# Optimization experiments

Measured on AMD Instinct MI355X. Metric: run time of the kernel, lower is better.

## Reference

```python
import jax, jax.numpy as jnp
import numpy as np

N_NODES = 50000
N_EDGES = 800000
H = 128   # atom_hidden_feats
B = 64    # bond_in_feats
NEG_SLOPE = 0.01  # torch LeakyReLU default


def setup_inputs() -> dict:
    key = jax.random.key(0)
    k1, k2, k3, k4, k5 = jax.random.split(key, 5)
    feat = jax.random.normal(k1, (N_NODES, H), dtype=jnp.float32)
    gdf_feat = jax.random.normal(k2, (N_EDGES, B), dtype=jnp.float32)
    # Linear(2H+B -> H): weight [H, 2H+B], bias [H]
    W = jax.random.normal(k3, (H, 2 * H + B), dtype=jnp.float32) * 0.05
    b = jnp.zeros((H,), dtype=jnp.float32)
    src = jax.random.randint(k4, (N_EDGES,), 0, N_NODES, dtype=jnp.int64)
    dst = jax.random.randint(k5, (N_EDGES,), 0, N_NODES, dtype=jnp.int64)
    return {"feat": feat, "gdf_feat": gdf_feat, "W": W, "b": b, "src": src, "dst": dst}


def reference(feat, gdf_feat, W, b, src, dst):
    n_nodes = feat.shape[0]
    # Per-edge message: concat(src_feat, dst_feat, edge_feat) -> linear -> gate
    z = jnp.concatenate([feat[src], feat[dst], gdf_feat], axis=-1)  # [E, 2H+B]
    z = z @ W.T + b                                                 # [E, H]
    msg = jax.nn.sigmoid(z) * jnp.where(z > 0, z, NEG_SLOPE * z)    # sigmoid * leaky_relu
    # Scatter-sum messages to destination nodes
    return jax.ops.segment_sum(msg, dst, num_segments=n_nodes)      # [N, H]
```

## Files before the change

### kernel.cpp

```cpp
#include <hip/hip_runtime.h>
#include <hip/hip_bf16.h>

typedef __attribute__((ext_vector_type(8)))  short bf16x8;
typedef __attribute__((ext_vector_type(16))) float f32x16;
typedef __attribute__((ext_vector_type(4)))  float f32x4;
typedef __attribute__((ext_vector_type(2)))  __fp16 fp16x2;

#define NN 50000
#define EE 800000
#define HH 128
#define KK 320
#define NEG 0.01f
#define NTILES (EE / 64)
#define NBLK 768
#define NSB 196

#define ACC_BYTES   ((size_t)NN * HH * 2)
#define FEATB_BYTES ((size_t)NN * HH * 2)
#define PERM_BYTES  ((size_t)EE * 4)
#define CNT_BYTES   ((size_t)50176 * 4)

__device__ __forceinline__ unsigned pack2(float a, float b) {
    unsigned short lo = __builtin_bit_cast(unsigned short, __float2bfloat16(a));
    unsigned short hi = __builtin_bit_cast(unsigned short, __float2bfloat16(b));
    return (unsigned)lo | ((unsigned)hi << 16);
}

__global__ __launch_bounds__(256) void featcvt_kernel(const float* __restrict__ feat,
                                                      ushort* __restrict__ featb)
{
    const int t = blockIdx.x * 256 + threadIdx.x;
    const float* p = feat + (long long)t * 8;
    f32x4 v0 = *(const f32x4*)p;
    f32x4 v1 = *(const f32x4*)(p + 4);
    int4 h;
    h.x = (int)pack2(v0[0], v0[1]); h.y = (int)pack2(v0[2], v0[3]);
    h.z = (int)pack2(v1[0], v1[1]); h.w = (int)pack2(v1[2], v1[3]);
    *(int4*)(featb + (long long)t * 8) = h;
}

__global__ __launch_bounds__(256) void hist_kernel(const int* __restrict__ dst,
                                                   unsigned* __restrict__ cnt)
{
    const int e = blockIdx.x * 256 + threadIdx.x;
    atomicAdd(&cnt[dst[e]], 1u);
}

__global__ __launch_bounds__(256) void scan1_kernel(const unsigned* __restrict__ cnt,
                                                    unsigned* __restrict__ base,
                                                    unsigned* __restrict__ bsum)
{
    __shared__ unsigned s[256];
    const int tid = threadIdx.x;
    const int g = blockIdx.x * 256 + tid;
    unsigned v = (g < NN) ? cnt[g] : 0u;
    s[tid] = v; __syncthreads();
    #pragma unroll
    for (int o = 1; o < 256; o <<= 1) {
        unsigned t = (tid >= o) ? s[tid - o] : 0u;
        __syncthreads();
        if (tid >= o) s[tid] += t;
        __syncthreads();
    }
    if (g < NN) base[g] = s[tid] - v;
    if (tid == 255) bsum[blockIdx.x] = s[255];
}

__global__ __launch_bounds__(256) void scan2_kernel(unsigned* __restrict__ bsum)
{
    __shared__ unsigned s[256];
    const int tid = threadIdx.x;
    unsigned v = (tid < NSB) ? bsum[tid] : 0u;
    s[tid] = v; __syncthreads();
    #pragma unroll
    for (int o = 1; o < 256; o <<= 1) {
        unsigned t = (tid >= o) ? s[tid - o] : 0u;
        __syncthreads();
        if (tid >= o) s[tid] += t;
        __syncthreads();
    }
    if (tid < NSB) bsum[tid] = s[tid] - v;
}

__global__ __launch_bounds__(256) void scan3_kernel(unsigned* __restrict__ base,
                                                    const unsigned* __restrict__ bsum)
{
    const int g = blockIdx.x * 256 + threadIdx.x;
    if (g < NN) base[g] += bsum[blockIdx.x];
}

__global__ __launch_bounds__(256) void permbuild_kernel(const int* __restrict__ dst,
                                                        const unsigned* __restrict__ base,
                                                        unsigned* __restrict__ cursor,
                                                        int* __restrict__ perm)
{
    const int e = blockIdx.x * 256 + threadIdx.x;
    const int d = dst[e];
    const unsigned rank = atomicAdd(&cursor[d], 1u);
    perm[base[d] + rank] = e;
}

__global__ __launch_bounds__(256, 3) void fused_sorted_kernel(
    const ushort* __restrict__ featb, const float* __restrict__ gdf,
    const float*  __restrict__ W,     const float* __restrict__ bias,
    const int*    __restrict__ src,   const int*   __restrict__ dst,
    const int*    __restrict__ perm,  __fp16* __restrict__ acc16)
{
    __shared__ char lds[64 * 640];
    __shared__ int  dsts[64];

    const int tid  = threadIdx.x;
    const int lane = tid & 63;
    const int wid  = tid >> 6;
    const int col  = wid * 32 + (lane & 31);
    const int khalf = lane >> 5;
    const int r = tid >> 2, q = tid & 3;

    bf16x8 Wb[20];
    {
        const float* wrow = W + col * KK + khalf * 8;
        #pragma unroll
        for (int k = 0; k < 20; k++) {
            f32x4 x0 = *(const f32x4*)(wrow + k * 16);
            f32x4 x1 = *(const f32x4*)(wrow + k * 16 + 4);
            union { bf16x8 v; unsigned u[4]; } t;
            t.u[0] = pack2(x0[0], x0[1]); t.u[1] = pack2(x0[2], x0[3]);
            t.u[2] = pack2(x1[0], x1[1]); t.u[3] = pack2(x1[2], x1[3]);
            Wb[k] = t.v;
        }
    }
    const float bv = bias[col];

    const int xcd = blockIdx.x & 7, wI = blockIdx.x >> 3;
    const int cid = xcd * (NBLK / 8) + wI;
    const int qc  = NTILES / NBLK;
    const int rem = NTILES % NBLK;
    const int t0  = cid * qc + (cid < rem ? cid : rem);
    const int len = qc + (cid < rem ? 1 : 0);

    int eCur, sCur, dCur;
    {
        const long long p = (long long)t0 * 64 + r;
        eCur = perm[p]; sCur = src[eCur]; dCur = dst[eCur];
    }

    const int arow = lane & 31;
    const int xa   = (arow & 7) << 4;

    auto flush = [&](int dn, float v) {
        const float o = __shfl_xor(v, 1);
        if (!(lane & 1)) {
            fp16x2 hv = __builtin_amdgcn_cvt_pkrtz(v, o);
            __fp16* pa = acc16 + (long long)dn * HH + col;
            asm volatile("global_atomic_pk_add_f16 %0, %1, off"
                         :: "v"(pa), "v"(hv) : "memory");
        }
    };

    for (int t = t0; t < t0 + len; ++t) {
        if (q == 0) dsts[r] = dCur;
        {
            const ushort* fs = featb + (long long)sCur * HH;
            const ushort* fd = featb + (long long)dCur * HH;
            const float*  ge = gdf + (long long)eCur * 64;
            const int xr = (r & 7) << 4;
            #pragma unroll
            for (int i = 0; i < 8; i++) {
                const int c = q + i * 4;
                int4 h = *(const int4*)((c < 16) ? (fs + c * 8) : (fd + (c - 16) * 8));
                *(int4*)(lds + r * 640 + ((c * 16) ^ xr)) = h;
            }
            #pragma unroll
            for (int i = 8; i < 10; i++) {
                const int c = q + i * 4;
                const float* p = ge + (c - 32) * 8;
                f32x4 v0 = *(const f32x4*)p;
                f32x4 v1 = *(const f32x4*)(p + 4);
                int4 h;
                h.x = (int)pack2(v0[0], v0[1]); h.y = (int)pack2(v0[2], v0[3]);
                h.z = (int)pack2(v1[0], v1[1]); h.w = (int)pack2(v1[2], v1[3]);
                *(int4*)(lds + r * 640 + ((c * 16) ^ xr)) = h;
            }
        }
        if (t + 1 < t0 + len) {
            const long long p = (long long)(t + 1) * 64 + r;
            eCur = perm[p]; sCur = src[eCur]; dCur = dst[eCur];
        }
        __syncthreads();

        f32x16 acc0 = {}; f32x16 acc1 = {};
        #pragma unroll
        for (int k = 0; k < 20; k++) {
            const int kb = k * 32 + khalf * 16;
            bf16x8 a0 = *(const bf16x8*)(lds + arow * 640 + (kb ^ xa));
            bf16x8 a1 = *(const bf16x8*)(lds + (arow + 32) * 640 + (kb ^ xa));
            acc0 = __builtin_amdgcn_mfma_f32_32x32x16_bf16(a0, Wb[k], acc0, 0, 0, 0);
            acc1 = __builtin_amdgcn_mfma_f32_32x32x16_bf16(a1, Wb[k], acc1, 0, 0, 0);
        }

        #pragma unroll
        for (int rt = 0; rt < 2; rt++) {
            const f32x16 A = rt ? acc1 : acc0;
            #pragma unroll
            for (int g = 0; g < 4; g++) {
                const int4 dn4 = *(const int4*)(&dsts[rt * 32 + g * 8 + khalf * 4]);
                const int dd[4] = { dn4.x, dn4.y, dn4.z, dn4.w };
                float mm[4];
                #pragma unroll
                for (int j = 0; j < 4; j++) {
                    const float z  = A[g * 4 + j] + bv;
                    const float lr = z > 0.f ? z : NEG * z;
                    mm[j] = lr / (1.f + __expf(-z));
                }
                float s = mm[0];
                #pragma unroll
                for (int j = 1; j < 4; j++) {
                    if (dd[j] == dd[j - 1]) s += mm[j];
                    else { flush(dd[j - 1], s); s = mm[j]; }
                }
                flush(dd[3], s);
            }
        }
        __syncthreads();
    }
}

__global__ __launch_bounds__(256) void conv_kernel(const int4* __restrict__ acc,
                                                   float4* __restrict__ out)
{
    const int i = blockIdx.x * 256 + threadIdx.x;
    union { int4 v; __fp16 h[8]; } u;
    u.v = acc[i];
    float4 a, b;
    a.x = (float)u.h[0]; a.y = (float)u.h[1]; a.z = (float)u.h[2]; a.w = (float)u.h[3];
    b.x = (float)u.h[4]; b.y = (float)u.h[5]; b.z = (float)u.h[6]; b.w = (float)u.h[7];
    out[2 * i]     = a;
    out[2 * i + 1] = b;
}

__global__ __launch_bounds__(256) void fused_fallback_kernel(
    const float* __restrict__ feat, const float* __restrict__ gdf,
    const float* __restrict__ W,    const float* __restrict__ bias,
    const int*   __restrict__ src,  const int*   __restrict__ dst,
    float* __restrict__ out)
{
    __shared__ int4 lds4[64 * 40];
    __shared__ int  dsts[64];
    char* lds = (char*)lds4;
    const int tid = threadIdx.x, lane = tid & 63, wid = tid >> 6;
    const int col = wid * 32 + (lane & 31), khalf = lane >> 5;
    const int r = tid >> 2, q = tid & 3;
    const long long ebase = (long long)blockIdx.x * 64;

    bf16x8 Wb[20];
    {
        const float* wrow = W + col * KK + khalf * 8;
        #pragma unroll
        for (int k = 0; k < 20; k++) {
            f32x4 x0 = *(const f32x4*)(wrow + k * 16);
            f32x4 x1 = *(const f32x4*)(wrow + k * 16 + 4);
            union { bf16x8 v; unsigned u[4]; } t;
            t.u[0] = pack2(x0[0], x0[1]); t.u[1] = pack2(x0[2], x0[3]);
            t.u[2] = pack2(x1[0], x1[1]); t.u[3] = pack2(x1[2], x1[3]);
            Wb[k] = t.v;
        }
    }
    const int s = src[ebase + r], d = dst[ebase + r];
    if (q == 0) dsts[r] = d;
    {
        const float* fs = feat + (long long)s * HH;
        const float* fd = feat + (long long)d * HH;
        const float* ge = gdf + (ebase + r) * 64;
        #pragma unroll
        for (int i = 0; i < 10; i++) {
            const int c = q + i * 4;
            const float* p = (c < 16) ? (fs + c * 8)
                           : (c < 32) ? (fd + (c - 16) * 8)
                                      : (ge + (c - 32) * 8);
            f32x4 v0 = *(const f32x4*)p;
            f32x4 v1 = *(const f32x4*)(p + 4);
            int4 h;
            h.x = (int)pack2(v0[0], v0[1]); h.y = (int)pack2(v0[2], v0[3]);
            h.z = (int)pack2(v1[0], v1[1]); h.w = (int)pack2(v1[2], v1[3]);
            *(int4*)(lds + r * 640 + ((c * 16) ^ ((r & 7) << 4))) = h;
        }
    }
    __syncthreads();
    f32x16 acc0 = {}; f32x16 acc1 = {};
    const int arow = lane & 31, xa = (arow & 7) << 4;
    #pragma unroll
    for (int k = 0; k < 20; k++) {
        const int kb = k * 32 + khalf * 16;
        bf16x8 a0 = *(const bf16x8*)(lds + arow * 640 + (kb ^ xa));
        bf16x8 a1 = *(const bf16x8*)(lds + (arow + 32) * 640 + (kb ^ xa));
        acc0 = __builtin_amdgcn_mfma_f32_32x32x16_bf16(a0, Wb[k], acc0, 0, 0, 0);
        acc1 = __builtin_amdgcn_mfma_f32_32x32x16_bf16(a1, Wb[k], acc1, 0, 0, 0);
    }
    const float bv = bias[col];
    #pragma unroll
    for (int rt = 0; rt < 2; rt++) {
        const f32x16 A = rt ? acc1 : acc0;
        #pragma unroll
        for (int g = 0; g < 4; g++) {
            #pragma unroll
            for (int j = 0; j < 4; j++) {
                const int reg = g * 4 + j;
                const int row = j + g * 8 + khalf * 4;
                const float z  = A[reg] + bv;
                const float lr = z > 0.f ? z : NEG * z;
                const float sgm = 1.f / (1.f + __expf(-z));
                unsafeAtomicAdd(out + (long long)dsts[rt * 32 + row] * HH + col, lr * sgm);
            }
        }
    }
}

extern "C" void kernel_launch(void* const* d_in, const int* in_sizes, int n_in,
                              void* d_out, int out_size, void* d_ws, size_t ws_size,
                              hipStream_t stream) {
    const float* feat = (const float*)d_in[0];
    const float* gdf  = (const float*)d_in[1];
    const float* W    = (const float*)d_in[2];
    const float* bias = (const float*)d_in[3];
    const int*   src  = (const int*)d_in[4];
    const int*   dst  = (const int*)d_in[5];
    float* out = (float*)d_out;

    char* wsb = (char*)d_ws;
    __fp16*   acc16  = (__fp16*)wsb;
    ushort*   featb  = (ushort*)(wsb + ACC_BYTES);
    int*      perm   = (int*)(wsb + ACC_BYTES + FEATB_BYTES);
    unsigned* cnt    = (unsigned*)(wsb + ACC_BYTES + FEATB_BYTES + PERM_BYTES);
    unsigned* base   = cnt + 50176;
    unsigned* cursor = base + 50176;
    unsigned* bsum   = cursor + 50176;
    const size_t fullBytes = ACC_BYTES + FEATB_BYTES + PERM_BYTES + 3 * CNT_BYTES + 4096;

    if (ws_size >= fullBytes) {
        (void)hipMemsetAsync(acc16, 0, ACC_BYTES, stream);
        (void)hipMemsetAsync(cnt, 0, CNT_BYTES, stream);
        (void)hipMemsetAsync(cursor, 0, CNT_BYTES + 4096, stream);
        featcvt_kernel<<<NN * HH / 8 / 256, 256, 0, stream>>>(feat, featb);
        hist_kernel<<<EE / 256, 256, 0, stream>>>(dst, cnt);
        scan1_kernel<<<NSB, 256, 0, stream>>>(cnt, base, bsum);
        scan2_kernel<<<1, 256, 0, stream>>>(bsum);
        scan3_kernel<<<NSB, 256, 0, stream>>>(base, bsum);
        permbuild_kernel<<<EE / 256, 256, 0, stream>>>(dst, base, cursor, perm);
        fused_sorted_kernel<<<NBLK, 256, 0, stream>>>(featb, gdf, W, bias,
                                                      src, dst, perm, acc16);
        conv_kernel<<<NN * HH / 8 / 256, 256, 0, stream>>>((const int4*)acc16,
                                                           (float4*)out);
    } else {
        (void)hipMemsetAsync(out, 0, (size_t)out_size * sizeof(float), stream);
        fused_fallback_kernel<<<EE / 64, 256, 0, stream>>>(feat, gdf, W, bias,
                                                           src, dst, out);
    }
}
```

Baseline: 359.9 us.

## Double-buffer edge tile staging and fuse histogram into feature conversion

The main sorted kernel now issues the global gathers for the next 64-edge tile into registers before running the MFMA loop on the current tile. It then writes them to LDS after the MFMAs, with a double-buffered destination index array, so gather latency overlaps compute. The histogram kernel is folded into the feature conversion kernel, since both have 800000 threads, and two memsets are merged into one, cutting launches. In exchange the kernel holds more registers for staged data, which may lower occupancy, and the single LDS tile buffer relies on barrier ordering for correctness.

```diff
diff --git a/kernel.cpp b/kernel.cpp
--- a/kernel.cpp
+++ b/kernel.cpp
@@ -26,8 +26,10 @@
     return (unsigned)lo | ((unsigned)hi << 16);
 }
 
-__global__ __launch_bounds__(256) void featcvt_kernel(const float* __restrict__ feat,
-                                                      ushort* __restrict__ featb)
+__global__ __launch_bounds__(256) void cvt_hist_kernel(const float* __restrict__ feat,
+                                                       ushort* __restrict__ featb,
+                                                       const int* __restrict__ dst,
+                                                       unsigned* __restrict__ cnt)
 {
     const int t = blockIdx.x * 256 + threadIdx.x;
     const float* p = feat + (long long)t * 8;
@@ -37,13 +39,7 @@
     h.x = (int)pack2(v0[0], v0[1]); h.y = (int)pack2(v0[2], v0[3]);
     h.z = (int)pack2(v1[0], v1[1]); h.w = (int)pack2(v1[2], v1[3]);
     *(int4*)(featb + (long long)t * 8) = h;
-}
-
-__global__ __launch_bounds__(256) void hist_kernel(const int* __restrict__ dst,
-                                                   unsigned* __restrict__ cnt)
-{
-    const int e = blockIdx.x * 256 + threadIdx.x;
-    atomicAdd(&cnt[dst[e]], 1u);
+    atomicAdd(&cnt[dst[t]], 1u);
 }
 
 __global__ __launch_bounds__(256) void scan1_kernel(const unsigned* __restrict__ cnt,
@@ -107,7 +103,7 @@
     const int*    __restrict__ perm,  __fp16* __restrict__ acc16)
 {
     __shared__ char lds[64 * 640];
-    __shared__ int  dsts[64];
+    __shared__ int  dsts[2][64];
 
     const int tid  = threadIdx.x;
     const int lane = tid & 63;
@@ -137,16 +133,47 @@
     const int rem = NTILES % NBLK;
     const int t0  = cid * qc + (cid < rem ? cid : rem);
     const int len = qc + (cid < rem ? 1 : 0);
-
-    int eCur, sCur, dCur;
-    {
-        const long long p = (long long)t0 * 64 + r;
-        eCur = perm[p]; sCur = src[eCur]; dCur = dst[eCur];
-    }
-
-    const int arow = lane & 31;
-    const int xa   = (arow & 7) << 4;
-
+    const int tEnd = t0 + len;
+
+    int4  sf[8];
+    f32x4 sgv[4];
+    int   dStage;
+
+    auto issueLoads = [&](int e_i, int s_i, int d_i) {
+        const ushort* fs = featb + (long long)s_i * HH;
+        const ushort* fd = featb + (long long)d_i * HH;
+        const float*  ge = gdf + (long long)e_i * 64;
+        #pragma unroll
+        for (int i = 0; i < 8; i++) {
+            const int c = q + i * 4;
+            sf[i] = *(const int4*)((c < 16) ? (fs + c * 8) : (fd + (c - 16) * 8));
+        }
+        #pragma unroll
+        for (int i = 0; i < 2; i++) {
+            const int cg = q + i * 4;
+            sgv[2 * i]     = *(const f32x4*)(ge + cg * 8);
+            sgv[2 * i + 1] = *(const f32x4*)(ge + cg * 8 + 4);
+        }
+    };
+    auto writeStage = [&](int buf) {
+        const int xr = (r & 7) << 4;
+        #pragma unroll
+        for (int i = 0; i < 8; i++) {
+            const int c = q + i * 4;
+            *(int4*)(lds + r * 640 + ((c * 16) ^ xr)) = sf[i];
+        }
+        #pragma unroll
+        for (int i = 0; i < 2; i++) {
+            const int c = 32 + q + i * 4;
+            int4 h;
+            h.x = (int)pack2(sgv[2*i][0], sgv[2*i][1]);
+            h.y = (int)pack2(sgv[2*i][2], sgv[2*i][3]);
+            h.z = (int)pack2(sgv[2*i+1][0], sgv[2*i+1][1]);
+            h.w = (int)pack2(sgv[2*i+1][2], sgv[2*i+1][3]);
+            *(int4*)(lds + r * 640 + ((c * 16) ^ xr)) = h;
+        }
+        if (q == 0) dsts[buf][r] = dStage;
+    };
     auto flush = [&](int dn, float v) {
         const float o = __shfl_xor(v, 1);
         if (!(lane & 1)) {
@@ -157,36 +184,36 @@
         }
     };
 
-    for (int t = t0; t < t0 + len; ++t) {
-        if (q == 0) dsts[r] = dCur;
-        {
-            const ushort* fs = featb + (long long)sCur * HH;
-            const ushort* fd = featb + (long long)dCur * HH;
-            const float*  ge = gdf + (long long)eCur * 64;
-            const int xr = (r & 7) << 4;
-            #pragma unroll
-            for (int i = 0; i < 8; i++) {
-                const int c = q + i * 4;
-                int4 h = *(const int4*)((c < 16) ? (fs + c * 8) : (fd + (c - 16) * 8));
-                *(int4*)(lds + r * 640 + ((c * 16) ^ xr)) = h;
+    int eA, sA, dA;
+    {
+        const long long p = (long long)t0 * 64 + r;
+        eA = perm[p]; sA = src[eA]; dA = dst[eA];
+    }
+    issueLoads(eA, sA, dA);
+    dStage = dA;
+    if (len > 1) {
+        const long long p = (long long)(t0 + 1) * 64 + r;
+        eA = perm[p]; sA = src[eA]; dA = dst[eA];
+    }
+    writeStage(0);
+    asm volatile("s_waitcnt lgkmcnt(0)" ::: "memory");
+    __builtin_amdgcn_sched_barrier(0);
+    __builtin_amdgcn_s_barrier();
+
+    const int arow = lane & 31;
+    const int xa   = (arow & 7) << 4;
+    int cur = 0;
+
+    for (int t = t0; ; ++t) {
+        const bool hasNext = (t + 1 < tEnd);
+        if (hasNext) {
+            issueLoads(eA, sA, dA);
+            dStage = dA;
+            if (t + 2 < tEnd) {
+                const long long p = (long long)(t + 2) * 64 + r;
+                eA = perm[p]; sA = src[eA]; dA = dst[eA];
             }
-            #pragma unroll
-            for (int i = 8; i < 10; i++) {
-                const int c = q + i * 4;
-                const float* p = ge + (c - 32) * 8;
-                f32x4 v0 = *(const f32x4*)p;
-                f32x4 v1 = *(const f32x4*)(p + 4);
-                int4 h;
-                h.x = (int)pack2(v0[0], v0[1]); h.y = (int)pack2(v0[2], v0[3]);
-                h.z = (int)pack2(v1[0], v1[1]); h.w = (int)pack2(v1[2], v1[3]);
-                *(int4*)(lds + r * 640 + ((c * 16) ^ xr)) = h;
-            }
-        }
-        if (t + 1 < t0 + len) {
-            const long long p = (long long)(t + 1) * 64 + r;
-            eCur = perm[p]; sCur = src[eCur]; dCur = dst[eCur];
-        }
-        __syncthreads();
+        }
 
         f32x16 acc0 = {}; f32x16 acc1 = {};
         #pragma unroll
@@ -198,12 +225,21 @@
             acc1 = __builtin_amdgcn_mfma_f32_32x32x16_bf16(a1, Wb[k], acc1, 0, 0, 0);
         }
 
+        if (hasNext) {
+            __builtin_amdgcn_s_barrier();
+            __builtin_amdgcn_sched_barrier(0);
+            writeStage(cur ^ 1);
+            asm volatile("s_waitcnt lgkmcnt(0)" ::: "memory");
+            __builtin_amdgcn_sched_barrier(0);
+            __builtin_amdgcn_s_barrier();
+        }
+
         #pragma unroll
         for (int rt = 0; rt < 2; rt++) {
             const f32x16 A = rt ? acc1 : acc0;
             #pragma unroll
             for (int g = 0; g < 4; g++) {
-                const int4 dn4 = *(const int4*)(&dsts[rt * 32 + g * 8 + khalf * 4]);
+                const int4 dn4 = *(const int4*)(&dsts[cur][rt * 32 + g * 8 + khalf * 4]);
                 const int dd[4] = { dn4.x, dn4.y, dn4.z, dn4.w };
                 float mm[4];
                 #pragma unroll
@@ -221,7 +257,9 @@
                 flush(dd[3], s);
             }
         }
-        __syncthreads();
+
+        if (!hasNext) break;
+        cur ^= 1;
     }
 }
 
@@ -331,17 +369,16 @@
     ushort*   featb  = (ushort*)(wsb + ACC_BYTES);
     int*      perm   = (int*)(wsb + ACC_BYTES + FEATB_BYTES);
     unsigned* cnt    = (unsigned*)(wsb + ACC_BYTES + FEATB_BYTES + PERM_BYTES);
-    unsigned* base   = cnt + 50176;
-    unsigned* cursor = base + 50176;
+    unsigned* cursor = cnt + 50176;
     unsigned* bsum   = cursor + 50176;
-    const size_t fullBytes = ACC_BYTES + FEATB_BYTES + PERM_BYTES + 3 * CNT_BYTES + 4096;
+    unsigned* base   = bsum + 1024;
+    const size_t fullBytes = ACC_BYTES + FEATB_BYTES + PERM_BYTES
+                           + 2 * CNT_BYTES + 4096 + CNT_BYTES;
 
     if (ws_size >= fullBytes) {
         (void)hipMemsetAsync(acc16, 0, ACC_BYTES, stream);
-        (void)hipMemsetAsync(cnt, 0, CNT_BYTES, stream);
-        (void)hipMemsetAsync(cursor, 0, CNT_BYTES + 4096, stream);
-        featcvt_kernel<<<NN * HH / 8 / 256, 256, 0, stream>>>(feat, featb);
-        hist_kernel<<<EE / 256, 256, 0, stream>>>(dst, cnt);
+        (void)hipMemsetAsync(cnt, 0, 2 * CNT_BYTES + 4096, stream);
+        cvt_hist_kernel<<<NN * HH / 8 / 256, 256, 0, stream>>>(feat, featb, dst, cnt);
         scan1_kernel<<<NSB, 256, 0, stream>>>(cnt, base, bsum);
         scan2_kernel<<<1, 256, 0, stream>>>(bsum);
         scan3_kernel<<<NSB, 256, 0, stream>>>(base, bsum);
```

After: 440.3 us. +22.3%, slower.

## Double-buffer async LDS tile loads and atomically accumulate fp32 directly into output

Applied to the files above, without the earlier changes.

The sorted fused kernel is rewritten to work on 32-edge tiles. Each tile's feature rows are prefetched with global_load_lds into a double-buffered LDS area while the current tile runs on MFMA, and index lookups are pipelined several tiles ahead. The fp16 packed-atomic accumulator, its memset, the run-merging of equal destinations and the final conversion kernel are removed; messages are now added straight into the fp32 output with per-element atomics. The feature conversion and the destination histogram are also merged into a single kernel. In exchange the kernel issues more global atomics per edge, because consecutive same-destination messages are no longer combined and fp32 atomics replace packed fp16 ones.

```diff
diff --git a/kernel.cpp b/kernel.cpp
--- a/kernel.cpp
+++ b/kernel.cpp
@@ -4,46 +4,45 @@
 typedef __attribute__((ext_vector_type(8)))  short bf16x8;
 typedef __attribute__((ext_vector_type(16))) float f32x16;
 typedef __attribute__((ext_vector_type(4)))  float f32x4;
-typedef __attribute__((ext_vector_type(2)))  __fp16 fp16x2;
 
 #define NN 50000
 #define EE 800000
 #define HH 128
 #define KK 320
 #define NEG 0.01f
-#define NTILES (EE / 64)
+#define TROWS 32
+#define NT2 (EE / TROWS)
 #define NBLK 768
 #define NSB 196
 
-#define ACC_BYTES   ((size_t)NN * HH * 2)
 #define FEATB_BYTES ((size_t)NN * HH * 2)
 #define PERM_BYTES  ((size_t)EE * 4)
-#define CNT_BYTES   ((size_t)50176 * 4)
-
-__device__ __forceinline__ unsigned pack2(float a, float b) {
+
+#define GLOAD_LDS(gp, lp) \
+    __builtin_amdgcn_global_load_lds( \
+        (const __attribute__((address_space(1))) void*)(gp), \
+        (__attribute__((address_space(3))) void*)(lp), 16, 0, 0)
+
+__device__ __forceinline__ int pack2(float a, float b) {
     unsigned short lo = __builtin_bit_cast(unsigned short, __float2bfloat16(a));
     unsigned short hi = __builtin_bit_cast(unsigned short, __float2bfloat16(b));
-    return (unsigned)lo | ((unsigned)hi << 16);
-}
-
-__global__ __launch_bounds__(256) void featcvt_kernel(const float* __restrict__ feat,
-                                                      ushort* __restrict__ featb)
+    return (int)((unsigned)lo | ((unsigned)hi << 16));
+}
+
+__global__ __launch_bounds__(256) void cvt_hist_kernel(const float* __restrict__ feat,
+                                                       ushort* __restrict__ featb,
+                                                       const int* __restrict__ dst,
+                                                       unsigned* __restrict__ cnt)
 {
     const int t = blockIdx.x * 256 + threadIdx.x;
     const float* p = feat + (long long)t * 8;
     f32x4 v0 = *(const f32x4*)p;
     f32x4 v1 = *(const f32x4*)(p + 4);
     int4 h;
-    h.x = (int)pack2(v0[0], v0[1]); h.y = (int)pack2(v0[2], v0[3]);
-    h.z = (int)pack2(v1[0], v1[1]); h.w = (int)pack2(v1[2], v1[3]);
+    h.x = pack2(v0[0], v0[1]); h.y = pack2(v0[2], v0[3]);
+    h.z = pack2(v1[0], v1[1]); h.w = pack2(v1[2], v1[3]);
     *(int4*)(featb + (long long)t * 8) = h;
-}
-
-__global__ __launch_bounds__(256) void hist_kernel(const int* __restrict__ dst,
-                                                   unsigned* __restrict__ cnt)
-{
-    const int e = blockIdx.x * 256 + threadIdx.x;
-    atomicAdd(&cnt[dst[e]], 1u);
+    atomicAdd(&cnt[dst[t]], 1u);
 }
 
 __global__ __launch_bounds__(256) void scan1_kernel(const unsigned* __restrict__ cnt,
@@ -100,21 +99,21 @@
     perm[base[d] + rank] = e;
 }
 
-__global__ __launch_bounds__(256, 3) void fused_sorted_kernel(
+__global__ __launch_bounds__(256, 3) void fused_async_kernel(
     const ushort* __restrict__ featb, const float* __restrict__ gdf,
     const float*  __restrict__ W,     const float* __restrict__ bias,
     const int*    __restrict__ src,   const int*   __restrict__ dst,
-    const int*    __restrict__ perm,  __fp16* __restrict__ acc16)
-{
-    __shared__ char lds[64 * 640];
-    __shared__ int  dsts[64];
+    const int*    __restrict__ perm,  float* __restrict__ out)
+{
+    __shared__ char lds[2][40 * 32 * 16];
+    __shared__ int  dsts[2][TROWS];
 
     const int tid  = threadIdx.x;
     const int lane = tid & 63;
     const int wid  = tid >> 6;
     const int col  = wid * 32 + (lane & 31);
     const int khalf = lane >> 5;
-    const int r = tid >> 2, q = tid & 3;
+    const int row  = lane & 31;
 
     bf16x8 Wb[20];
     {
@@ -123,7 +122,7 @@
         for (int k = 0; k < 20; k++) {
             f32x4 x0 = *(const f32x4*)(wrow + k * 16);
             f32x4 x1 = *(const f32x4*)(wrow + k * 16 + 4);
-            union { bf16x8 v; unsigned u[4]; } t;
+            union { bf16x8 v; int u[4]; } t;
             t.u[0] = pack2(x0[0], x0[1]); t.u[1] = pack2(x0[2], x0[3]);
             t.u[2] = pack2(x1[0], x1[1]); t.u[3] = pack2(x1[2], x1[3]);
             Wb[k] = t.v;
@@ -133,109 +132,109 @@
 
     const int xcd = blockIdx.x & 7, wI = blockIdx.x >> 3;
     const int cid = xcd * (NBLK / 8) + wI;
-    const int qc  = NTILES / NBLK;
-    const int rem = NTILES % NBLK;
+    const int qc  = NT2 / NBLK;
+    const int rem = NT2 % NBLK;
     const int t0  = cid * qc + (cid < rem ? cid : rem);
     const int len = qc + (cid < rem ? 1 : 0);
-
-    int eCur, sCur, dCur;
-    {
-        const long long p = (long long)t0 * 64 + r;
-        eCur = perm[p]; sCur = src[eCur]; dCur = dst[eCur];
-    }
-
-    const int arow = lane & 31;
-    const int xa   = (arow & 7) << 4;
-
-    auto flush = [&](int dn, float v) {
-        const float o = __shfl_xor(v, 1);
-        if (!(lane & 1)) {
-            fp16x2 hv = __builtin_amdgcn_cvt_pkrtz(v, o);
-            __fp16* pa = acc16 + (long long)dn * HH + col;
-            asm volatile("global_atomic_pk_add_f16 %0, %1, off"
-                         :: "v"(pa), "v"(hv) : "memory");
-        }
-    };
-
-    for (int t = t0; t < t0 + len; ++t) {
-        if (q == 0) dsts[r] = dCur;
+    const int tEnd = t0 + len;
+
+    {
+        const int e0 = perm[(long long)t0 * TROWS + row];
+        const int s0 = src[e0], d0 = dst[e0];
+        #pragma unroll
+        for (int i = 0; i < 4; i++) {
+            const int cb = wid * 8 + i * 2;
+            const int c  = cb + khalf;
+            const ushort* g = (c < 16) ? featb + (size_t)s0 * HH + c * 8
+                                       : featb + (size_t)d0 * HH + (c - 16) * 8;
+            GLOAD_LDS(g, &lds[0][cb * 512]);
+        }
+        const float* ge = gdf + (size_t)e0 * 64 + (wid * 2 + khalf) * 8;
+        f32x4 g0 = *(const f32x4*)ge;
+        f32x4 g1 = *(const f32x4*)(ge + 4);
+        int4 h;
+        h.x = pack2(g0[0], g0[1]); h.y = pack2(g0[2], g0[3]);
+        h.z = pack2(g1[0], g1[1]); h.w = pack2(g1[2], g1[3]);
+        *(int4*)(&lds[0][((32 + wid * 2 + khalf) * 32 + row) * 16]) = h;
+        if (wid == 0 && khalf == 0) dsts[0][row] = d0;
+    }
+    int eA, sA, dA, eB;
+    {
+        const int tA = (t0 + 1 < tEnd) ? t0 + 1 : t0;
+        eA = perm[(long long)tA * TROWS + row];
+        sA = src[eA]; dA = dst[eA];
+        const int tB = (t0 + 2 < tEnd) ? t0 + 2 : t0;
+        eB = perm[(long long)tB * TROWS + row];
+    }
+    asm volatile("s_waitcnt vmcnt(0) lgkmcnt(0)" ::: "memory");
+    __builtin_amdgcn_sched_barrier(0);
+    __builtin_amdgcn_s_barrier();
+    __builtin_amdgcn_sched_barrier(0);
+
+    int buf = 0;
+    for (int t = t0; ; ++t) {
+        const bool hasNext = (t + 1 < tEnd);
+        f32x4 g0, g1;
+        if (hasNext) {
+            #pragma unroll
+            for (int i = 0; i < 4; i++) {
+                const int cb = wid * 8 + i * 2;
+                const int c  = cb + khalf;
+                const ushort* g = (c < 16) ? featb + (size_t)sA * HH + c * 8
+                                           : featb + (size_t)dA * HH + (c - 16) * 8;
+                GLOAD_LDS(g, &lds[buf ^ 1][cb * 512]);
+            }
+            const float* ge = gdf + (size_t)eA * 64 + (wid * 2 + khalf) * 8;
+            g0 = *(const f32x4*)ge;
+            g1 = *(const f32x4*)(ge + 4);
+            if (wid == 0 && khalf == 0) dsts[buf ^ 1][row] = dA;
+        }
+        __builtin_amdgcn_sched_barrier(0);
+        int sB = sA, dB = dA, eC = eB;
+        if (hasNext) {
+            sB = src[eB]; dB = dst[eB];
+            const int tC = (t + 3 < tEnd) ? t + 3 : t0;
+            eC = perm[(long long)tC * TROWS + row];
+        }
+        __builtin_amdgcn_sched_barrier(0);
+
+        f32x16 acc = {};
+        #pragma unroll
+        for (int k = 0; k < 20; k++) {
+            bf16x8 a = *(const bf16x8*)(&lds[buf][((2 * k + khalf) * 32 + row) * 16]);
+            acc = __builtin_amdgcn_mfma_f32_32x32x16_bf16(a, Wb[k], acc, 0, 0, 0);
+        }
+
+        __builtin_amdgcn_sched_barrier(0);
+        #pragma unroll
+        for (int g = 0; g < 4; g++) {
+            const int4 dn4 = *(const int4*)(&dsts[buf][g * 8 + khalf * 4]);
+            const int dd[4] = { dn4.x, dn4.y, dn4.z, dn4.w };
+            #pragma unroll
+            for (int j = 0; j < 4; j++) {
+                const float z  = acc[g * 4 + j] + bv;
+                const float lr = z > 0.f ? z : NEG * z;
+                const float m  = lr / (1.f + __expf(-z));
+                unsafeAtomicAdd(out + (size_t)dd[j] * HH + col, m);
+            }
+        }
+        __builtin_amdgcn_sched_barrier(0);
+
+        if (!hasNext) break;
         {
-            const ushort* fs = featb + (long long)sCur * HH;
-            const ushort* fd = featb + (long long)dCur * HH;
-            const float*  ge = gdf + (long long)eCur * 64;
-            const int xr = (r & 7) << 4;
-            #pragma unroll
-            for (int i = 0; i < 8; i++) {
-                const int c = q + i * 4;
-                int4 h = *(const int4*)((c < 16) ? (fs + c * 8) : (fd + (c - 16) * 8));
-                *(int4*)(lds + r * 640 + ((c * 16) ^ xr)) = h;
-            }
-            #pragma unroll
-            for (int i = 8; i < 10; i++) {
-                const int c = q + i * 4;
-                const float* p = ge + (c - 32) * 8;
-                f32x4 v0 = *(const f32x4*)p;
-                f32x4 v1 = *(const f32x4*)(p + 4);
-                int4 h;
-                h.x = (int)pack2(v0[0], v0[1]); h.y = (int)pack2(v0[2], v0[3]);
-                h.z = (int)pack2(v1[0], v1[1]); h.w = (int)pack2(v1[2], v1[3]);
-                *(int4*)(lds + r * 640 + ((c * 16) ^ xr)) = h;
-            }
-        }
-        if (t + 1 < t0 + len) {
-            const long long p = (long long)(t + 1) * 64 + r;
-            eCur = perm[p]; sCur = src[eCur]; dCur = dst[eCur];
-        }
-        __syncthreads();
-
-        f32x16 acc0 = {}; f32x16 acc1 = {};
-        #pragma unroll
-        for (int k = 0; k < 20; k++) {
-            const int kb = k * 32 + khalf * 16;
-            bf16x8 a0 = *(const bf16x8*)(lds + arow * 640 + (kb ^ xa));
-            bf16x8 a1 = *(const bf16x8*)(lds + (arow + 32) * 640 + (kb ^ xa));
-            acc0 = __builtin_amdgcn_mfma_f32_32x32x16_bf16(a0, Wb[k], acc0, 0, 0, 0);
-            acc1 = __builtin_amdgcn_mfma_f32_32x32x16_bf16(a1, Wb[k], acc1, 0, 0, 0);
-        }
-
-        #pragma unroll
-        for (int rt = 0; rt < 2; rt++) {
-            const f32x16 A = rt ? acc1 : acc0;
-            #pragma unroll
-            for (int g = 0; g < 4; g++) {
-                const int4 dn4 = *(const int4*)(&dsts[rt * 32 + g * 8 + khalf * 4]);
-                const int dd[4] = { dn4.x, dn4.y, dn4.z, dn4.w };
-                float mm[4];
-                #pragma unroll
-                for (int j = 0; j < 4; j++) {
-                    const float z  = A[g * 4 + j] + bv;
-                    const float lr = z > 0.f ? z : NEG * z;
-                    mm[j] = lr / (1.f + __expf(-z));
-                }
-                float s = mm[0];
-                #pragma unroll
-                for (int j = 1; j < 4; j++) {
-                    if (dd[j] == dd[j - 1]) s += mm[j];
-                    else { flush(dd[j - 1], s); s = mm[j]; }
-                }
-                flush(dd[3], s);
-            }
-        }
-        __syncthreads();
-    }
-}
-
-__global__ __launch_bounds__(256) void conv_kernel(const int4* __restrict__ acc,
-                                                   float4* __restrict__ out)
-{
-    const int i = blockIdx.x * 256 + threadIdx.x;
-    union { int4 v; __fp16 h[8]; } u;
-    u.v = acc[i];
-    float4 a, b;
-    a.x = (float)u.h[0]; a.y = (float)u.h[1]; a.z = (float)u.h[2]; a.w = (float)u.h[3];
-    b.x = (float)u.h[4]; b.y = (float)u.h[5]; b.z = (float)u.h[6]; b.w = (float)u.h[7];
-    out[2 * i]     = a;
-    out[2 * i + 1] = b;
+            int4 h;
+            h.x = pack2(g0[0], g0[1]); h.y = pack2(g0[2], g0[3]);
+            h.z = pack2(g1[0], g1[1]); h.w = pack2(g1[2], g1[3]);
+            *(int4*)(&lds[buf ^ 1][((32 + wid * 2 + khalf) * 32 + row) * 16]) = h;
+        }
+        __builtin_amdgcn_sched_barrier(0);
+        asm volatile("s_waitcnt vmcnt(21) lgkmcnt(0)" ::: "memory");
+        __builtin_amdgcn_sched_barrier(0);
+        __builtin_amdgcn_s_barrier();
+        __builtin_amdgcn_sched_barrier(0);
+        eA = eB; sA = sB; dA = dB; eB = eC;
+        buf ^= 1;
+    }
 }
 
 __global__ __launch_bounds__(256) void fused_fallback_kernel(
@@ -259,7 +258,7 @@
         for (int k = 0; k < 20; k++) {
             f32x4 x0 = *(const f32x4*)(wrow + k * 16);
             f32x4 x1 = *(const f32x4*)(wrow + k * 16 + 4);
-            union { bf16x8 v; unsigned u[4]; } t;
+            union { bf16x8 v; int u[4]; } t;
             t.u[0] = pack2(x0[0], x0[1]); t.u[1] = pack2(x0[2], x0[3]);
             t.u[2] = pack2(x1[0], x1[1]); t.u[3] = pack2(x1[2], x1[3]);
             Wb[k] = t.v;
@@ -280,8 +279,8 @@
             f32x4 v0 = *(const f32x4*)p;
             f32x4 v1 = *(const f32x4*)(p + 4);
             int4 h;
-            h.x = (int)pack2(v0[0], v0[1]); h.y = (int)pack2(v0[2], v0[3]);
-            h.z = (int)pack2(v1[0], v1[1]); h.w = (int)pack2(v1[2], v1[3]);
+            h.x = pack2(v0[0], v0[1]); h.y = pack2(v0[2], v0[3]);
+            h.z = pack2(v1[0], v1[1]); h.w = pack2(v1[2], v1[3]);
             *(int4*)(lds + r * 640 + ((c * 16) ^ ((r & 7) << 4))) = h;
         }
     }
@@ -305,11 +304,11 @@
             #pragma unroll
             for (int j = 0; j < 4; j++) {
                 const int reg = g * 4 + j;
-                const int row = j + g * 8 + khalf * 4;
+                const int rw = j + g * 8 + khalf * 4;
                 const float z  = A[reg] + bv;
                 const float lr = z > 0.f ? z : NEG * z;
                 const float sgm = 1.f / (1.f + __expf(-z));
-                unsafeAtomicAdd(out + (long long)dsts[rt * 32 + row] * HH + col, lr * sgm);
+                unsafeAtomicAdd(out + (long long)dsts[rt * 32 + rw] * HH + col, lr * sgm);
             }
         }
     }
@@ -327,29 +326,24 @@
     float* out = (float*)d_out;
 
     char* wsb = (char*)d_ws;
-    __fp16*   acc16  = (__fp16*)wsb;
-    ushort*   featb  = (ushort*)(wsb + ACC_BYTES);
-    int*      perm   = (int*)(wsb + ACC_BYTES + FEATB_BYTES);
-    unsigned* cnt    = (unsigned*)(wsb + ACC_BYTES + FEATB_BYTES + PERM_BYTES);
-    unsigned* base   = cnt + 50176;
-    unsigned* cursor = base + 50176;
+    ushort*   featb  = (ushort*)wsb;
+    int*      perm   = (int*)(wsb + FEATB_BYTES);
+    unsigned* cnt    = (unsigned*)(wsb + FEATB_BYTES + PERM_BYTES);
+    unsigned* cursor = cnt + 50176;
     unsigned* bsum   = cursor + 50176;
-    const size_t fullBytes = ACC_BYTES + FEATB_BYTES + PERM_BYTES + 3 * CNT_BYTES + 4096;
+    unsigned* base   = bsum + 1024;
+    const size_t fullBytes = FEATB_BYTES + PERM_BYTES + (3 * 50176 + 1024) * 4;
 
     if (ws_size >= fullBytes) {
-        (void)hipMemsetAsync(acc16, 0, ACC_BYTES, stream);
-        (void)hipMemsetAsync(cnt, 0, CNT_BYTES, stream);
-        (void)hipMemsetAsync(cursor, 0, CNT_BYTES + 4096, stream);
-        featcvt_kernel<<<NN * HH / 8 / 256, 256, 0, stream>>>(feat, featb);
-        hist_kernel<<<EE / 256, 256, 0, stream>>>(dst, cnt);
+        (void)hipMemsetAsync(out, 0, (size_t)out_size * sizeof(float), stream);
+        (void)hipMemsetAsync(cnt, 0, (2 * 50176 + 1024) * 4, stream);
+        cvt_hist_kernel<<<NN * HH / 8 / 256, 256, 0, stream>>>(feat, featb, dst, cnt);
         scan1_kernel<<<NSB, 256, 0, stream>>>(cnt, base, bsum);
         scan2_kernel<<<1, 256, 0, stream>>>(bsum);
         scan3_kernel<<<NSB, 256, 0, stream>>>(base, bsum);
         permbuild_kernel<<<EE / 256, 256, 0, stream>>>(dst, base, cursor, perm);
-        fused_sorted_kernel<<<NBLK, 256, 0, stream>>>(featb, gdf, W, bias,
-                                                      src, dst, perm, acc16);
-        conv_kernel<<<NN * HH / 8 / 256, 256, 0, stream>>>((const int4*)acc16,
-                                                           (float4*)out);
+        fused_async_kernel<<<NBLK, 256, 0, stream>>>(featb, gdf, W, bias,
+                                                     src, dst, perm, out);
     } else {
         (void)hipMemsetAsync(out, 0, (size_t)out_size * sizeof(float), stream);
         fused_fallback_kernel<<<EE / 64, 256, 0, stream>>>(feat, gdf, W, bias,
```

Measured after the change: 1.197 ms. 233% more time.
